# Kernel optimization log

Hardware: AMD Instinct MI355X
Metric: run time of the kernel (lower is better)

The kernel has to match this reference:

```python
import jax, jax.numpy as jnp
import numpy as np

B = 4
N = 300000
GRIDS = [(64, 48, 8), (32, 24, 4), (16, 12, 2), (8, 6, 1)]
W_IMG = 640
EFF_R = 2.0 * (int(0.01 * W_IMG + 2) / W_IMG)  # 0.025, as in source
MAXV = [EFF_R, 2.0 * EFF_R, 2.0 / 24.0, 2.0 / 12.0, 2.0 / 6.0]
CIN = [3, 18, 66, 130, 130]
COUT = [16, 64, 128, 128, 128]
E_CNT = [3600000, 786432, 196608, 24576, 3072]
V_CNT = [N, 98304, 12288, 1536, 192]


def cartesian(pos, src, dst, max_value):
    # PyG Cartesian(norm=True, cat=False, max_value=mv) followed by clamp(0,1)
    cart = pos[dst] - pos[src]
    return jnp.clip(cart / (2.0 * max_value) + 0.5, 0.0, 1.0)


def spline_conv(x, src, dst, pseudo, Wk, Wr, b, num_nodes):
    # SplineConv, kernel_size=2, degree=1 B-spline over 3-D pseudo coords:
    # 8 corner weights, per-edge trilinear basis, mean aggregation + root + bias.
    p, q = pseudo, 1.0 - pseudo
    xs = x[src]  # [E, Cin] gather
    msg = jnp.zeros((src.shape[0], Wk.shape[-1]), x.dtype)
    for s in range(8):
        basis = ((p[:, 0] if s & 1 else q[:, 0])
                 * (p[:, 1] if s & 2 else q[:, 1])
                 * (p[:, 2] if s & 4 else q[:, 2]))
        msg = msg + basis[:, None] * (xs @ Wk[s])
    agg = jax.ops.segment_sum(msg, dst, num_segments=num_nodes)
    deg = jax.ops.segment_sum(jnp.ones((dst.shape[0],), x.dtype), dst, num_segments=num_nodes)
    out = agg / jnp.maximum(deg, 1.0)[:, None] + x @ Wr + b
    return jax.nn.relu(out)


def voxel_pool(x, pos, batch, grid, aggr):
    nx, ny, nt = grid
    ix = jnp.clip(jnp.floor(pos[:, 0] * nx).astype(jnp.int32), 0, nx - 1)
    iy = jnp.clip(jnp.floor(pos[:, 1] * ny).astype(jnp.int32), 0, ny - 1)
    it = jnp.clip(jnp.floor(pos[:, 2] * nt).astype(jnp.int32), 0, nt - 1)
    cluster = ((batch * nx + ix) * ny + iy) * nt + it
    V = B * nx * ny * nt
    ones = jnp.ones((x.shape[0],), x.dtype)
    cnt = jax.ops.segment_sum(ones, cluster, num_segments=V)
    posp = jax.ops.segment_sum(pos, cluster, num_segments=V) / jnp.maximum(cnt, 1.0)[:, None]
    if aggr == 'max':
        xp = jax.ops.segment_max(x, cluster, num_segments=V)
        xp = jnp.where(cnt[:, None] > 0, xp, 0.0)
    else:
        xp = jax.ops.segment_sum(x, cluster, num_segments=V) / jnp.maximum(cnt, 1.0)[:, None]
    batchp = jnp.arange(V, dtype=jnp.int32) // (nx * ny * nt)
    return xp, posp, batchp


def _forward(x, pos, batch, edges, params):
    e0 = edges[0]
    ea = cartesian(pos, e0[0], e0[1], MAXV[0])
    h = jnp.concatenate([x, pos[:, :2]], axis=1)
    Wk, Wr, bb = params[0]
    h = spline_conv(h, e0[0], e0[1], ea, Wk, Wr, bb, x.shape[0])
    h, pos, batch = voxel_pool(h, pos, batch, GRIDS[0], 'max')
    out3 = None
    for i in range(4):
        e = edges[i + 1]
        ea = cartesian(pos, e[0], e[1], MAXV[i + 1])
        h = jnp.concatenate([h, pos[:, :2]], axis=1)
        Wk, Wr, bb = params[i + 1]
        h = spline_conv(h, e[0], e[1], ea, Wk, Wr, bb, pos.shape[0])
        if i == 2:
            out3 = h  # features after layer4 (out3 scale)
        if i < 3:
            h, pos, batch = voxel_pool(h, pos, batch, GRIDS[i + 1], 'max' if i < 2 else 'mean')
    return out3, h


def setup_inputs() -> dict:
    key = jax.random.key(0)
    ks = jax.random.split(key, 40)
    inp = {}
    inp['x'] = jax.random.uniform(ks[0], (N, 1), dtype=jnp.float32)
    inp['pos'] = jax.random.uniform(ks[1], (N, 3), dtype=jnp.float32)
    inp['batch'] = jnp.sort(jax.random.randint(ks[2], (N,), 0, B, dtype=jnp.int32))
    for i in range(5):
        inp[f'e{i}'] = jax.random.randint(ks[3 + i], (2, E_CNT[i]), 0, V_CNT[i], dtype=jnp.int32)
    kidx = 8
    for i in range(5):
        scale = 1.0 / np.sqrt(8.0 * CIN[i])
        inp[f'W{i + 1}'] = scale * jax.random.normal(ks[kidx], (8, CIN[i], COUT[i]), dtype=jnp.float32); kidx += 1
        inp[f'R{i + 1}'] = scale * jax.random.normal(ks[kidx], (CIN[i], COUT[i]), dtype=jnp.float32); kidx += 1
        inp[f'b{i + 1}'] = jnp.zeros((COUT[i],), dtype=jnp.float32)
    return inp


def reference(x, pos, batch, e0, e1, e2, e3, e4,
              W1, R1, b1, W2, R2, b2, W3, R3, b3, W4, R4, b4, W5, R5, b5):
    params = [(W1, R1, b1), (W2, R2, b2), (W3, R3, b3), (W4, R4, b4), (W5, R5, b5)]
    edges = [e0, e1, e2, e3, e4]
    return _forward(x, pos, batch, edges, params)
```

## Files before the change

kernel.cpp:

```cpp
#include <hip/hip_runtime.h>
#include <cstdint>

__device__ __forceinline__ float clamp01f(float v) { return fminf(fmaxf(v, 0.0f), 1.0f); }

__device__ __forceinline__ void basis8(float p0, float p1, float p2, float* bs)
{
    float q0 = 1.f - p0, q1 = 1.f - p1, q2 = 1.f - p2;
    float t00 = q0 * q1, t10 = p0 * q1, t01 = q0 * p1, t11 = p0 * p1;
    bs[0] = t00 * q2; bs[1] = t10 * q2; bs[2] = t01 * q2; bs[3] = t11 * q2;
    bs[4] = t00 * p2; bs[5] = t10 * p2; bs[6] = t01 * p2; bs[7] = t11 * p2;
}

__global__ __launch_bounds__(256) void edge_count_kernel(
    const int* __restrict__ edst, int* __restrict__ cnt, int E)
{
    int e = blockIdx.x * 256 + threadIdx.x;
    if (e < E) atomicAdd(&cnt[__builtin_nontemporal_load(&edst[e])], 1);
}

__global__ __launch_bounds__(256) void edge_scatter_kernel(
    const int* __restrict__ esrc, const int* __restrict__ edst,
    int* __restrict__ off, int* __restrict__ srcs, int E, int rv)
{
    const int lo = (int)(blockIdx.x & 7) * rv;
    const int hi = lo + rv;
    const int base = (int)(blockIdx.x >> 3) << 10;
#pragma unroll
    for (int k = 0; k < 4; ++k) {
        int e = base + (k << 8) + threadIdx.x;
        if (e < E) {
            int d = __builtin_nontemporal_load(&edst[e]);
            if (d >= lo && d < hi) {
                int s = __builtin_nontemporal_load(&esrc[e]);
                int slot = atomicAdd(&off[d], 1);
                srcs[slot] = s;
            }
        }
    }
}

__global__ __launch_bounds__(256) void scan1_kernel(
    const int* __restrict__ cnt, int* __restrict__ off, int* __restrict__ bsum, int V)
{
    __shared__ int lds[4096];
    __shared__ int ssum[256];
    const int t = threadIdx.x;
    const int base = blockIdx.x * 4096;
    for (int i = t; i < 4096; i += 256) {
        int g = base + i;
        lds[i] = (g < V) ? cnt[g] : 0;
    }
    __syncthreads();
    int loc[16];
    int s = 0;
#pragma unroll
    for (int k = 0; k < 16; ++k) { loc[k] = s; s += lds[t * 16 + k]; }
    ssum[t] = s;
    __syncthreads();
    for (int d = 1; d < 256; d <<= 1) {
        int v = (t >= d) ? ssum[t - d] : 0;
        __syncthreads();
        ssum[t] += v;
        __syncthreads();
    }
    const int tbase = (t == 0) ? 0 : ssum[t - 1];
    if (t == 255 && bsum) bsum[blockIdx.x] = ssum[255];
#pragma unroll
    for (int k = 0; k < 16; ++k) lds[t * 16 + k] = tbase + loc[k];
    __syncthreads();
    for (int i = t; i < 4096; i += 256) {
        int g = base + i;
        if (g < V) off[g] = lds[i];
    }
}

__global__ __launch_bounds__(256) void scan_add_kernel(
    int* __restrict__ off, const int* __restrict__ bso, int V)
{
    int g = blockIdx.x * 256 + threadIdx.x;
    if (g < V) off[g] += bso[g >> 12];
}

__global__ __launch_bounds__(256) void bin_count_kernel(
    const int* __restrict__ edst, int* __restrict__ gcnt, int E, int shift)
{
    __shared__ int h[256];
    const int t = threadIdx.x;
    h[t] = 0;
    __syncthreads();
    const int base = blockIdx.x << 12;
#pragma unroll
    for (int k = 0; k < 16; ++k) {
        int e = base + (k << 8) + t;
        if (e < E) {
            int d = __builtin_nontemporal_load(&edst[e]);
            atomicAdd(&h[d >> shift], 1);
        }
    }
    __syncthreads();
    if (h[t]) atomicAdd(&gcnt[t], h[t]);
}

__global__ __launch_bounds__(256) void bin_scatter_kernel(
    const int* __restrict__ esrc, const int* __restrict__ edst,
    int* __restrict__ gcur, int2* __restrict__ st, int E, int shift)
{
    __shared__ int d_l[4096];
    __shared__ int s_l[4096];
    __shared__ int h[256];
    __shared__ int rbase[256];
    const int t = threadIdx.x;
    h[t] = 0;
    __syncthreads();
    const int base = blockIdx.x << 12;
#pragma unroll
    for (int k = 0; k < 16; ++k) {
        int i = (k << 8) + t;
        int e = base + i;
        if (e < E) {
            int d = __builtin_nontemporal_load(&edst[e]);
            int s = __builtin_nontemporal_load(&esrc[e]);
            d_l[i] = d; s_l[i] = s;
            atomicAdd(&h[d >> shift], 1);
        }
    }
    __syncthreads();
    rbase[t] = h[t] ? atomicAdd(&gcur[t], h[t]) : 0;
    h[t] = 0;
    __syncthreads();
#pragma unroll
    for (int k = 0; k < 16; ++k) {
        int i = (k << 8) + t;
        int e = base + i;
        if (e < E) {
            int d = d_l[i];
            int b = d >> shift;
            int r = atomicAdd(&h[b], 1);
            st[rbase[b] + r] = make_int2(d, s_l[i]);
        }
    }
}

__global__ __launch_bounds__(1024) void bucket_csr_kernel(
    const int* __restrict__ gcur, const int* __restrict__ gcnt,
    const int2* __restrict__ st,
    int* __restrict__ cnt, int* __restrict__ off, int* __restrict__ srcs,
    int V, int shift)
{
    __shared__ int h[2048];
    __shared__ int o[2048];
    __shared__ int ps[1024];
    const int t = threadIdx.x;
    const int b = blockIdx.x;
    const int v0 = b << shift;
    const int nv = min(1 << shift, V - v0);
    const int s1 = gcur[b];
    const int s0 = s1 - gcnt[b];
    h[t] = 0; h[t + 1024] = 0;
    __syncthreads();
    for (int i = s0 + t; i < s1; i += 1024)
        atomicAdd(&h[st[i].x - v0], 1);
    __syncthreads();
    int a = h[2 * t], b2 = h[2 * t + 1];
    ps[t] = a + b2;
    __syncthreads();
    for (int d = 1; d < 1024; d <<= 1) {
        int v = (t >= d) ? ps[t - d] : 0;
        __syncthreads();
        ps[t] += v;
        __syncthreads();
    }
    int pb = (t == 0) ? 0 : ps[t - 1];
    o[2 * t] = pb;
    o[2 * t + 1] = pb + a;
    __syncthreads();
    for (int i = t; i < nv; i += 1024) {
        int hv = h[i];
        cnt[v0 + i] = hv;
        off[v0 + i] = s0 + o[i] + hv;
    }
    __syncthreads();
    for (int i = s0 + t; i < s1; i += 1024) {
        int2 e = st[i];
        int r = atomicAdd(&o[e.x - v0], 1);
        srcs[s0 + r] = e.y;
    }
}

__global__ __launch_bounds__(256) void pack_xpos_kernel(
    const float* __restrict__ x, const float* __restrict__ pos,
    float4* __restrict__ xp, int V)
{
    int n = blockIdx.x * 256 + threadIdx.x;
    if (n >= V) return;
    xp[n] = make_float4(x[n], pos[n * 3 + 0], pos[n * 3 + 1], pos[n * 3 + 2]);
}

__device__ __forceinline__ void l1_edge_acc(
    const float4 d, const float4 a, float inv2mv, float ts[8][3])
{
    float p0 = clamp01f((d.y - a.y) * inv2mv + 0.5f);
    float p1 = clamp01f((d.z - a.z) * inv2mv + 0.5f);
    float p2 = clamp01f((d.w - a.w) * inv2mv + 0.5f);
    float bs[8];
    basis8(p0, p1, p2, bs);
#pragma unroll
    for (int s8 = 0; s8 < 8; ++s8) {
        ts[s8][0] += bs[s8] * a.x;
        ts[s8][1] += bs[s8] * a.y;
        ts[s8][2] += bs[s8] * a.z;
    }
}

__global__ __launch_bounds__(256) void l1_fused_kernel(
    const int* __restrict__ off, const int* __restrict__ cnt, const int* __restrict__ srcs,
    const float4* __restrict__ xp,
    const float* __restrict__ Wk, const float* __restrict__ Wr,
    const float* __restrict__ bias, float* __restrict__ out,
    float inv2mv, int V)
{
    __shared__ float sWk[384];
    __shared__ float sWr[48];
    __shared__ float sB[16];
    const int t = threadIdx.x;
    for (int i = t; i < 384; i += 256) sWk[i] = Wk[i];
    if (t < 48) sWr[t] = Wr[t];
    if (t < 16) sB[t] = bias[t];
    __syncthreads();
    const int v = blockIdx.x * 256 + t;
    if (v >= V) return;
    const float4 d = xp[v];
    const int e1 = off[v];
    const int n = cnt[v];
    float ts[8][3];
#pragma unroll
    for (int s8 = 0; s8 < 8; ++s8) { ts[s8][0] = 0.f; ts[s8][1] = 0.f; ts[s8][2] = 0.f; }
    int j = e1 - n;
    for (; j + 3 < e1; j += 4) {
        float4 a0 = xp[srcs[j]];
        float4 a1 = xp[srcs[j + 1]];
        float4 a2 = xp[srcs[j + 2]];
        float4 a3 = xp[srcs[j + 3]];
        l1_edge_acc(d, a0, inv2mv, ts);
        l1_edge_acc(d, a1, inv2mv, ts);
        l1_edge_acc(d, a2, inv2mv, ts);
        l1_edge_acc(d, a3, inv2mv, ts);
    }
    for (; j < e1; ++j)
        l1_edge_acc(d, xp[srcs[j]], inv2mv, ts);
    const float invn = 1.0f / fmaxf((float)n, 1.0f);
    float rr[16];
#pragma unroll
    for (int c = 0; c < 16; ++c) {
        float m = 0.f;
#pragma unroll
        for (int s8 = 0; s8 < 8; ++s8)
            m += ts[s8][0] * sWk[s8 * 48 + c]
               + ts[s8][1] * sWk[s8 * 48 + 16 + c]
               + ts[s8][2] * sWk[s8 * 48 + 32 + c];
        float r = m * invn + d.x * sWr[c] + d.y * sWr[16 + c] + d.z * sWr[32 + c] + sB[c];
        rr[c] = fmaxf(r, 0.0f);
    }
    float4* op = (float4*)(out + (size_t)v * 16);
#pragma unroll
    for (int k = 0; k < 4; ++k)
        op[k] = make_float4(rr[4 * k], rr[4 * k + 1], rr[4 * k + 2], rr[4 * k + 3]);
}

__device__ __forceinline__ void l2_edge_acc(
    const float4 pd, const float4 pa, float fa, int l16, float inv2mv,
    float* accF, float* accP)
{
    float p0 = clamp01f((pd.x - pa.x) * inv2mv + 0.5f);
    float p1 = clamp01f((pd.y - pa.y) * inv2mv + 0.5f);
    float p2 = clamp01f((pd.z - pa.z) * inv2mv + 0.5f);
    float bs[8];
    basis8(p0, p1, p2, bs);
    const float fp = (l16 == 0) ? pa.x : ((l16 == 1) ? pa.y : 0.f);
#pragma unroll
    for (int s8 = 0; s8 < 8; ++s8) {
        accF[s8] += bs[s8] * fa;
        accP[s8] += bs[s8] * fp;
    }
}

template<int NW>
__global__ __launch_bounds__(64 * NW) void tsum16_layer_kernel(
    const int* __restrict__ off, const int* __restrict__ cnt, const int* __restrict__ srcs,
    const float4* __restrict__ pos4, const float* __restrict__ feat,
    const float* __restrict__ Wk, const float* __restrict__ Wr,
    const float* __restrict__ bias, float* __restrict__ out,
    float inv2mv, int V)
{
    __shared__ float tsum[NW][4][18][9];
    const int tid = threadIdx.x;
    const int w = tid >> 6, lane = tid & 63;
    const int q = lane >> 4, l16 = lane & 15;
    const int vbase = (blockIdx.x * NW + w) * 4;
    const int v = vbase + q;

    const float4 pd = pos4[v];
    const int e1 = off[v];
    const int n = cnt[v];
    float accF[8], accP[8];
#pragma unroll
    for (int s8 = 0; s8 < 8; ++s8) { accF[s8] = 0.f; accP[s8] = 0.f; }
    int j = e1 - n;
    for (; j + 3 < e1; j += 4) {
        const int s0 = srcs[j], s1 = srcs[j + 1], s2 = srcs[j + 2], s3 = srcs[j + 3];
        const float4 pa = pos4[s0];
        const float4 pb = pos4[s1];
        const float4 pc = pos4[s2];
        const float4 pe = pos4[s3];
        const float fa = feat[s0 * 16 + l16];
        const float fb = feat[s1 * 16 + l16];
        const float fc = feat[s2 * 16 + l16];
        const float fe = feat[s3 * 16 + l16];
        l2_edge_acc(pd, pa, fa, l16, inv2mv, accF, accP);
        l2_edge_acc(pd, pb, fb, l16, inv2mv, accF, accP);
        l2_edge_acc(pd, pc, fc, l16, inv2mv, accF, accP);
        l2_edge_acc(pd, pe, fe, l16, inv2mv, accF, accP);
    }
    for (; j < e1; ++j) {
        const int s = srcs[j];
        const float4 pa = pos4[s];
        const float fa = feat[s * 16 + l16];
        l2_edge_acc(pd, pa, fa, l16, inv2mv, accF, accP);
    }
#pragma unroll
    for (int s8 = 0; s8 < 8; ++s8)
        tsum[w][q][l16][s8] = accF[s8];
    tsum[w][q][l16][8] = feat[v * 16 + l16];
    if (l16 < 2) {
#pragma unroll
        for (int s8 = 0; s8 < 8; ++s8)
            tsum[w][q][16 + l16][s8] = accP[s8];
        tsum[w][q][16 + l16][8] = (l16 == 0) ? pd.x : pd.y;
    }
    __syncthreads();

    float oA[4], oR[4];
#pragma unroll
    for (int b = 0; b < 4; ++b) { oA[b] = 0.f; oR[b] = 0.f; }
    for (int s8 = 0; s8 < 8; ++s8) {
        const float* W = Wk + (size_t)s8 * 18 * 64;
        for (int ci = 0; ci < 18; ++ci) {
            float wv = W[ci * 64 + lane];
#pragma unroll
            for (int b = 0; b < 4; ++b)
                oA[b] += tsum[w][b][ci][s8] * wv;
        }
    }
    for (int ci = 0; ci < 18; ++ci) {
        float wv = Wr[ci * 64 + lane];
#pragma unroll
        for (int b = 0; b < 4; ++b)
            oR[b] += tsum[w][b][ci][8] * wv;
    }
    const float bi = bias[lane];
#pragma unroll
    for (int b = 0; b < 4; ++b) {
        int vv = vbase + b;
        float invn = 1.0f / fmaxf((float)cnt[vv], 1.0f);
        out[(size_t)vv * 64 + lane] = fmaxf(oA[b] * invn + oR[b] + bi, 0.0f);
    }
}

template<int CINF, int COUT, int NV, int NW, int PMODE>
__global__ __launch_bounds__(64 * NW) void tsum_layer_kernel(
    const int* __restrict__ off, const int* __restrict__ cnt, const int* __restrict__ srcs,
    const float4* __restrict__ pos4, const float* __restrict__ feat,
    const float* __restrict__ Wk, const float* __restrict__ Wr,
    const float* __restrict__ bias, float* __restrict__ out,
    float* __restrict__ hp, float* __restrict__ psum, float* __restrict__ pcnt,
    float inv2mv, int V, int gx, int gy, int gt, int bdiv)
{
    constexpr int CIN = CINF + 2;
    constexpr int NCI = (CIN + 63) / 64;
    constexpr int NCC = COUT / 64;
    __shared__ float tsum[NW][NV][CIN][9];
    __shared__ int scl[NW][NV];
    const int tid = threadIdx.x;
    const int w = tid >> 6, lane = tid & 63;
    const int vbase = (blockIdx.x * NW + w) * NV;

    for (int b = 0; b < NV; ++b) {
        const int v = vbase + b;
        if (v >= V) break;
        const float4 pd = pos4[v];
        float acc[NCI][8];
#pragma unroll
        for (int k = 0; k < NCI; ++k)
#pragma unroll
            for (int s8 = 0; s8 < 8; ++s8) acc[k][s8] = 0.f;
        const int e1 = off[v];
        int j = e1 - cnt[v];
        for (; j + 1 < e1; j += 2) {
            const int s0 = srcs[j], s1 = srcs[j + 1];
            const float4 pa = pos4[s0];
            const float4 pb = pos4[s1];
            float fa[NCI], fb[NCI];
#pragma unroll
            for (int k = 0; k < NCI; ++k) {
                int ci = lane + 64 * k;
                fa[k] = (ci < CINF) ? feat[s0 * CINF + ci]
                       : (ci == CINF ? pa.x : (ci == CINF + 1 ? pa.y : 0.f));
                fb[k] = (ci < CINF) ? feat[s1 * CINF + ci]
                       : (ci == CINF ? pb.x : (ci == CINF + 1 ? pb.y : 0.f));
            }
            float pa0 = clamp01f((pd.x - pa.x) * inv2mv + 0.5f);
            float pa1 = clamp01f((pd.y - pa.y) * inv2mv + 0.5f);
            float pa2 = clamp01f((pd.z - pa.z) * inv2mv + 0.5f);
            float pb0 = clamp01f((pd.x - pb.x) * inv2mv + 0.5f);
            float pb1 = clamp01f((pd.y - pb.y) * inv2mv + 0.5f);
            float pb2 = clamp01f((pd.z - pb.z) * inv2mv + 0.5f);
            float ba[8], bb[8];
            basis8(pa0, pa1, pa2, ba);
            basis8(pb0, pb1, pb2, bb);
#pragma unroll
            for (int s8 = 0; s8 < 8; ++s8)
#pragma unroll
                for (int k = 0; k < NCI; ++k)
                    acc[k][s8] += ba[s8] * fa[k] + bb[s8] * fb[k];
        }
        if (j < e1) {
            const int s = srcs[j];
            const float4 pa = pos4[s];
            float fa[NCI];
#pragma unroll
            for (int k = 0; k < NCI; ++k) {
                int ci = lane + 64 * k;
                fa[k] = (ci < CINF) ? feat[s * CINF + ci]
                       : (ci == CINF ? pa.x : (ci == CINF + 1 ? pa.y : 0.f));
            }
            float p0 = clamp01f((pd.x - pa.x) * inv2mv + 0.5f);
            float p1 = clamp01f((pd.y - pa.y) * inv2mv + 0.5f);
            float p2 = clamp01f((pd.z - pa.z) * inv2mv + 0.5f);
            float bs[8];
            basis8(p0, p1, p2, bs);
#pragma unroll
            for (int s8 = 0; s8 < 8; ++s8)
#pragma unroll
                for (int k = 0; k < NCI; ++k)
                    acc[k][s8] += bs[s8] * fa[k];
        }
#pragma unroll
        for (int k = 0; k < NCI; ++k) {
            int ci = lane + 64 * k;
            if (ci < CIN) {
#pragma unroll
                for (int s8 = 0; s8 < 8; ++s8)
                    tsum[w][b][ci][s8] = acc[k][s8];
                tsum[w][b][ci][8] = (ci < CINF) ? feat[v * CINF + ci]
                                                : (ci == CINF ? pd.x : pd.y);
            }
        }
        if (PMODE != 0 && lane == 0) {
            int bb2 = v / bdiv;
            int ix = min(max((int)floorf(pd.x * (float)gx), 0), gx - 1);
            int iy = min(max((int)floorf(pd.y * (float)gy), 0), gy - 1);
            int it = min(max((int)floorf(pd.z * (float)gt), 0), gt - 1);
            int cl = ((bb2 * gx + ix) * gy + iy) * gt + it;
            scl[w][b] = cl;
            atomicAdd(&psum[cl * 3 + 0], pd.x);
            atomicAdd(&psum[cl * 3 + 1], pd.y);
            atomicAdd(&psum[cl * 3 + 2], pd.z);
            atomicAdd(&pcnt[cl], 1.0f);
        }
    }
    __syncthreads();

    float oA[NV][NCC], oR[NV][NCC];
#pragma unroll
    for (int b = 0; b < NV; ++b)
#pragma unroll
        for (int cc = 0; cc < NCC; ++cc) { oA[b][cc] = 0.f; oR[b][cc] = 0.f; }
    for (int s8 = 0; s8 < 8; ++s8) {
        const float* W = Wk + (size_t)s8 * CIN * COUT;
        for (int ci = 0; ci < CIN; ++ci) {
            float wv[NCC];
#pragma unroll
            for (int cc = 0; cc < NCC; ++cc)
                wv[cc] = W[(size_t)ci * COUT + cc * 64 + lane];
#pragma unroll
            for (int b = 0; b < NV; ++b) {
                float tv = tsum[w][b][ci][s8];
#pragma unroll
                for (int cc = 0; cc < NCC; ++cc) oA[b][cc] += tv * wv[cc];
            }
        }
    }
    for (int ci = 0; ci < CIN; ++ci) {
        float wv[NCC];
#pragma unroll
        for (int cc = 0; cc < NCC; ++cc)
            wv[cc] = Wr[(size_t)ci * COUT + cc * 64 + lane];
#pragma unroll
        for (int b = 0; b < NV; ++b) {
            float tv = tsum[w][b][ci][8];
#pragma unroll
            for (int cc = 0; cc < NCC; ++cc) oR[b][cc] += tv * wv[cc];
        }
    }
    for (int b = 0; b < NV; ++b) {
        int v = vbase + b;
        if (v >= V) break;
        float invn = 1.0f / fmaxf((float)cnt[v], 1.0f);
#pragma unroll
        for (int cc = 0; cc < NCC; ++cc) {
            int c = cc * 64 + lane;
            float val = fmaxf(oA[b][cc] * invn + oR[b][cc] + bias[c], 0.0f);
            if (PMODE == 0 || PMODE == 2)
                out[(size_t)v * COUT + c] = val;
            if (PMODE == 1)
                atomicMax((int*)&hp[(size_t)scl[w][b] * COUT + c], __float_as_int(val));
            if (PMODE == 2)
                atomicAdd(&hp[(size_t)scl[w][b] * COUT + c], val);
        }
    }
}

__global__ __launch_bounds__(256) void pool_cluster_kernel(
    const float* __restrict__ p4, int ofs, const int* __restrict__ batch, int bdiv, int V,
    int nx, int ny, int nt, int* __restrict__ cl, int* __restrict__ cnt)
{
    int n = blockIdx.x * 256 + threadIdx.x;
    if (n >= V) return;
    int b = batch ? batch[n] : (n / bdiv);
    const float* pp = p4 + (size_t)n * 4 + ofs;
    float px = pp[0], py = pp[1], pt = pp[2];
    int ix = (int)floorf(px * (float)nx); ix = min(max(ix, 0), nx - 1);
    int iy = (int)floorf(py * (float)ny); iy = min(max(iy, 0), ny - 1);
    int it = (int)floorf(pt * (float)nt); it = min(max(it, 0), nt - 1);
    int c = ((b * nx + ix) * ny + iy) * nt + it;
    cl[n] = c;
    atomicAdd(&cnt[c], 1);
}

__global__ __launch_bounds__(256) void pool_scatter_kernel(
    const int* __restrict__ cl, int* __restrict__ off, int* __restrict__ order, int V, int rv)
{
    const int lo = (int)(blockIdx.x & 7) * rv;
    const int hi = lo + rv;
    const int base = (int)(blockIdx.x >> 3) << 10;
#pragma unroll
    for (int k = 0; k < 4; ++k) {
        int n = base + (k << 8) + threadIdx.x;
        if (n < V) {
            int c = __builtin_nontemporal_load(&cl[n]);
            if (c >= lo && c < hi) {
                int slot = atomicAdd(&off[c], 1);
                order[slot] = n;
            }
        }
    }
}

template<int COUT>
__global__ __launch_bounds__(256) void staged_pool_kernel(
    const int* __restrict__ order, const int* __restrict__ cl,
    const int* __restrict__ ioff, const int* __restrict__ icnt,
    const float* __restrict__ h, const float* __restrict__ p4, int ofs,
    float* __restrict__ hp, float* __restrict__ psum, int V)
{
    __shared__ float sh[256][COUT + 4];
    __shared__ float sp[256][3];
    __shared__ int scl2[256];
    const int t = threadIdx.x;
    const int w = t >> 6, lane = t & 63;
    const int gbase = blockIdx.x * 256 + w * 64;
    const int slot = gbase + lane;
    int myc = -1;
    if (slot < V) {
        int n = order[slot];
        myc = cl[n];
        const float* hr = h + (size_t)n * COUT;
#pragma unroll
        for (int k = 0; k < COUT / 4; ++k)
            *(float4*)&sh[w * 64 + lane][k * 4] = *(const float4*)&hr[k * 4];
        const float* pp = p4 + (size_t)n * 4 + ofs;
        sp[w * 64 + lane][0] = pp[0];
        sp[w * 64 + lane][1] = pp[1];
        sp[w * 64 + lane][2] = pp[2];
    }
    scl2[w * 64 + lane] = myc;
    __syncthreads();

    if (lane < COUT) {
        const int c = lane;
        const int sb = w * 64;
        int prev = scl2[sb];
        float run = 0.f, rp = 0.f;
        for (int i = 0; i < 64; ++i) {
            int cc = scl2[sb + i];
            if (cc != prev) {
                if (prev >= 0) {
                    int en = ioff[prev];
                    int st = en - icnt[prev];
                    if (st >= gbase && en <= gbase + 64) {
                        hp[(size_t)prev * COUT + c] = run;
                        if (c < 3) psum[prev * 3 + c] = rp;
                    } else {
                        atomicMax((int*)&hp[(size_t)prev * COUT + c], __float_as_int(run));
                        if (c < 3) atomicAdd(&psum[prev * 3 + c], rp);
                    }
                }
                prev = cc; run = 0.f; rp = 0.f;
            }
            if (cc >= 0) {
                run = fmaxf(run, sh[sb + i][c]);
                if (c < 3) rp += sp[sb + i][c];
            }
        }
        if (prev >= 0) {
            int en = ioff[prev];
            int st = en - icnt[prev];
            if (st >= gbase && en <= gbase + 64) {
                hp[(size_t)prev * COUT + c] = run;
                if (c < 3) psum[prev * 3 + c] = rp;
            } else {
                atomicMax((int*)&hp[(size_t)prev * COUT + c], __float_as_int(run));
                if (c < 3) atomicAdd(&psum[prev * 3 + c], rp);
            }
        }
    }
}

__global__ __launch_bounds__(256) void finalize_posI_kernel(
    const float* __restrict__ psum, const int* __restrict__ icnt,
    float4* __restrict__ pos_out, int Vc)
{
    int c = blockIdx.x * 256 + threadIdx.x;
    if (c >= Vc) return;
    float m = fmaxf((float)icnt[c], 1.0f);
    pos_out[c] = make_float4(psum[c * 3 + 0] / m, psum[c * 3 + 1] / m,
                             psum[c * 3 + 2] / m, 0.f);
}

__global__ __launch_bounds__(256) void finalize_pos_kernel(
    const float* __restrict__ psum, const float* __restrict__ pcnt,
    float4* __restrict__ pos_out, int Vc)
{
    int c = blockIdx.x * 256 + threadIdx.x;
    if (c >= Vc) return;
    float m = fmaxf(pcnt[c], 1.0f);
    pos_out[c] = make_float4(psum[c * 3 + 0] / m, psum[c * 3 + 1] / m,
                             psum[c * 3 + 2] / m, 0.f);
}

__global__ __launch_bounds__(256) void finalize_mean_kernel(
    const float* __restrict__ hsum, const float* __restrict__ psum,
    const float* __restrict__ pcnt,
    float* __restrict__ hout, float4* __restrict__ pos_out, int Vc)
{
    int g = blockIdx.x * 256 + threadIdx.x;
    if (g >= Vc * 128) return;
    int c = g >> 7, ch = g & 127;
    float m = fmaxf(pcnt[c], 1.0f);
    hout[g] = hsum[g] / m;
    if (ch == 0)
        pos_out[c] = make_float4(psum[c * 3 + 0] / m, psum[c * 3 + 1] / m,
                                 psum[c * 3 + 2] / m, 0.f);
}

extern "C" void kernel_launch(void* const* d_in, const int* in_sizes, int n_in,
                              void* d_out, int out_size, void* d_ws, size_t ws_size,
                              hipStream_t stream)
{
    (void)in_sizes; (void)n_in; (void)out_size;
    const float* x    = (const float*)d_in[0];
    const float* pos0 = (const float*)d_in[1];
    const int*   bat  = (const int*)d_in[2];
    const int* e1 = (const int*)d_in[3];
    const int* e2 = (const int*)d_in[4];
    const int* e3 = (const int*)d_in[5];
    const int* e4 = (const int*)d_in[6];
    const int* e5 = (const int*)d_in[7];
    const float* W1 = (const float*)d_in[8],  *R1 = (const float*)d_in[9],  *B1 = (const float*)d_in[10];
    const float* W2 = (const float*)d_in[11], *R2 = (const float*)d_in[12], *B2 = (const float*)d_in[13];
    const float* W3 = (const float*)d_in[14], *R3 = (const float*)d_in[15], *B3 = (const float*)d_in[16];
    const float* W4 = (const float*)d_in[17], *R4 = (const float*)d_in[18], *B4 = (const float*)d_in[19];
    const float* W5 = (const float*)d_in[20], *R5 = (const float*)d_in[21], *B5 = (const float*)d_in[22];

    const int E1 = 3600000, E2 = 786432, E3 = 196608, E4 = 24576, E5 = 3072;

    if (ws_size < (size_t)21800000 * sizeof(float)) return;
    float* ws = (float*)d_ws;
    float* P0 = ws;
    float* P1 = ws + 12600000;
    float* P2 = ws + 18900000;
    int*   P3 = (int*)(ws + 20500000);
    float* P4 = ws + 21500000;
    int* GCNT   = P3 + 990000;
    int* GCUR   = P3 + 990256;
    int* SCR_BS = P3 + 999744;
    int* SCR_BO = SCR_BS + 96;

    float* out3 = (float*)d_out;
    float* hfin = (float*)d_out + 196608;

#define MSI(p, ni) hipMemsetAsync((p), 0, (size_t)(ni) * sizeof(int), stream)

#define SCAN(cntp, offp, Vn)                                                                     \
    {                                                                                            \
        int nb_ = ((Vn) + 4095) / 4096;                                                          \
        if (nb_ <= 1) {                                                                          \
            scan1_kernel<<<1, 256, 0, stream>>>((cntp), (offp), nullptr, (Vn));                  \
        } else {                                                                                 \
            scan1_kernel<<<nb_, 256, 0, stream>>>((cntp), (offp), SCR_BS, (Vn));                 \
            scan1_kernel<<<1, 256, 0, stream>>>(SCR_BS, SCR_BO, nullptr, nb_);                   \
            scan_add_kernel<<<((Vn) + 255) / 256, 256, 0, stream>>>((offp), SCR_BO, (Vn));       \
        }                                                                                        \
    }

#define BSORT(cntP, offP, srcP, stP, ep, En, Vn, SHIFT, NB)                                      \
    {                                                                                            \
        MSI(GCNT, 256);                                                                          \
        bin_count_kernel<<<((En) + 4095) / 4096, 256, 0, stream>>>((ep) + (En), GCNT, En, SHIFT);\
        scan1_kernel<<<1, 256, 0, stream>>>(GCNT, GCUR, nullptr, NB);                            \
        bin_scatter_kernel<<<((En) + 4095) / 4096, 256, 0, stream>>>(                            \
            (ep), (ep) + (En), GCUR, stP, En, SHIFT);                                            \
        bucket_csr_kernel<<<NB, 1024, 0, stream>>>(                                              \
            GCUR, GCNT, stP, cntP, offP, srcP, Vn, SHIFT);                                       \
    }

#define ESORT(base, ep, En, Vn)                                                                  \
    int* cnt_ = (base);                                                                          \
    int* off_ = cnt_ + (Vn);                                                                     \
    int* src_ = off_ + (Vn);                                                                     \
    MSI(cnt_, (Vn));                                                                             \
    edge_count_kernel<<<((En) + 255) / 256, 256, 0, stream>>>((ep) + (En), cnt_, En);            \
    SCAN(cnt_, off_, (Vn));                                                                      \
    edge_scatter_kernel<<<8 * (((En) + 1023) / 1024), 256, 0, stream>>>(                         \
        (ep), (ep) + (En), off_, src_, En, (Vn) >> 3)

#define SPOOL(ICLp, IORDp, ICNTp, IOFFp, p4src, ofsv, batp, bdiv, Vn, Vc, NX, NY, NT, COUTV, \
              hsrc, hpool, psumP, posdst)                                                   \
    {                                                                                       \
        MSI(ICNTp, (Vc));                                                                   \
        pool_cluster_kernel<<<((Vn) + 255) / 256, 256, 0, stream>>>(                        \
            p4src, ofsv, batp, bdiv, Vn, NX, NY, NT, ICLp, ICNTp);                          \
        SCAN(ICNTp, IOFFp, (Vc));                                                           \
        pool_scatter_kernel<<<8 * (((Vn) + 1023) / 1024), 256, 0, stream>>>(                \
            ICLp, IOFFp, IORDp, Vn, (Vc) >> 3);                                             \
        MSI(hpool, (size_t)(Vc) * (COUTV));                                                 \
        MSI(psumP, (size_t)(Vc) * 3);                                                       \
        staged_pool_kernel<COUTV><<<((Vn) + 255) / 256, 256, 0, stream>>>(                  \
            IORDp, ICLp, IOFFp, ICNTp, hsrc, p4src, ofsv, hpool, psumP, Vn);                \
        finalize_posI_kernel<<<((Vc) + 255) / 256, 256, 0, stream>>>(                       \
            psumP, ICNTp, (float4*)(posdst), Vc);                                           \
    }

    {
        int* cnt1 = (int*)P0;
        int* off1 = cnt1 + 300000;
        int* src1 = off1 + 300000;
        int2* st1 = (int2*)(src1 + 3600000);
        float4* xp4 = (float4*)(P0 + 11400000);
        BSORT(cnt1, off1, src1, st1, e1, E1, 300000, 11, 147);
        pack_xpos_kernel<<<(300000 + 255) / 256, 256, 0, stream>>>(x, pos0, xp4, 300000);
        l1_fused_kernel<<<(300000 + 255) / 256, 256, 0, stream>>>(
            off1, cnt1, src1, xp4, W1, R1, B1, P1, 20.0f, 300000);
        int* ICL1  = P3;
        int* IORD1 = P3 + 300000;
        int* ICNT1 = P3 + 600000;
        int* IOFF1 = P3 + 698304;
        SPOOL(ICL1, IORD1, ICNT1, IOFF1, (const float*)xp4, 1, bat, 0, 300000, 98304,
              64, 48, 8, 16, P1, P2, P0, P0 + 300000);
    }
    float4* pos2_4 = (float4*)(P0 + 300000);
    {
        int* cnt2 = P3;
        int* off2 = cnt2 + 98304;
        int* src2 = off2 + 98304;
        int2* st2 = (int2*)(P0 + 1000000);
        BSORT(cnt2, off2, src2, st2, e2, E2, 98304, 10, 96);
        tsum16_layer_kernel<4><<<98304 / 16, 256, 0, stream>>>(
            off2, cnt2, src2, pos2_4, P2, W2, R2, B2, P1, 10.0f, 98304);
        int* ICL2  = P3;
        int* IORD2 = P3 + 98304;
        int* ICNT2 = P3 + 196608;
        int* IOFF2 = P3 + 208896;
        SPOOL(ICL2, IORD2, ICNT2, IOFF2, (const float*)pos2_4, 0, nullptr, 24576,
              98304, 12288, 32, 24, 4, 64, P1, P2, P2 + 786432, P4);
    }
    {
        ESORT(P3, e3, E3, 12288);
        float* HP3 = P1;
        float* PS3 = P1 + 196608;
        float* PC3 = P1 + 201216;
        MSI(P1, 202752);
        tsum_layer_kernel<64, 128, 4, 4, 1><<<12288 / 16, 256, 0, stream>>>(
            off_, cnt_, src_, (const float4*)P4, P2, W3, R3, B3, nullptr,
            HP3, PS3, PC3, 6.0f, 12288, 16, 12, 2, 3072);
        finalize_pos_kernel<<<(1536 + 255) / 256, 256, 0, stream>>>(
            PS3, PC3, (float4*)P0, 1536);
    }
    {
        ESORT(P3, e4, E4, 1536);
        float* HS4 = P2;
        float* PS4 = P2 + 24576;
        float* PC4 = P2 + 25152;
        MSI(P2, 25344);
        tsum_layer_kernel<128, 128, 2, 4, 2><<<1536 / 8, 256, 0, stream>>>(
            off_, cnt_, src_, (const float4*)P0, P1, W4, R4, B4, out3,
            HS4, PS4, PC4, 3.0f, 1536, 8, 6, 1, 384);
        finalize_mean_kernel<<<(192 * 128 + 255) / 256, 256, 0, stream>>>(
            HS4, PS4, PC4, P1, (float4*)(P0 + 100000), 192);
    }
    {
        ESORT(P3, e5, E5, 192);
        tsum_layer_kernel<128, 128, 2, 4, 0><<<192 / 8, 256, 0, stream>>>(
            off_, cnt_, src_, (const float4*)(P0 + 100000), P1, W5, R5, B5, hfin,
            nullptr, nullptr, nullptr, 1.5f, 192, 1, 1, 1, 1);
    }
#undef SPOOL
#undef ESORT
#undef BSORT
#undef SCAN
#undef MSI
}
```

Before: 840.9 us.

## Fuse voxel cluster assignment into conv kernels and simplify pseudo-coordinate math

Drops the separate pool_cluster_kernel. Voxel cluster ids and counts are now computed at the end of the layer-1 and layer-2 spline conv kernels, and buffers are relocated so layer 2 does not overwrite the sort buffers. Per-edge pseudo-coordinate math is rewritten as a precomputed destination offset plus one FMA, and the clamp uses fmed3. This saves two launches and a re-read of positions, at the cost of extra atomics inside the conv kernels and slightly different floating-point rounding.

```diff
diff --git a/kernel.cpp b/kernel.cpp
--- a/kernel.cpp
+++ b/kernel.cpp
@@ -1,7 +1,10 @@
 #include <hip/hip_runtime.h>
 #include <cstdint>
 
-__device__ __forceinline__ float clamp01f(float v) { return fminf(fmaxf(v, 0.0f), 1.0f); }
+__device__ __forceinline__ float clamp01f(float v)
+{
+    return __builtin_amdgcn_fmed3f(v, 0.0f, 1.0f);
+}
 
 __device__ __forceinline__ void basis8(float p0, float p1, float p2, float* bs)
 {
@@ -197,11 +200,11 @@
 }
 
 __device__ __forceinline__ void l1_edge_acc(
-    const float4 d, const float4 a, float inv2mv, float ts[8][3])
-{
-    float p0 = clamp01f((d.y - a.y) * inv2mv + 0.5f);
-    float p1 = clamp01f((d.z - a.z) * inv2mv + 0.5f);
-    float p2 = clamp01f((d.w - a.w) * inv2mv + 0.5f);
+    float dx_, float dy_, float dz_, const float4 a, float inv2mv, float ts[8][3])
+{
+    float p0 = clamp01f(fmaf(-inv2mv, a.y, dx_));
+    float p1 = clamp01f(fmaf(-inv2mv, a.z, dy_));
+    float p2 = clamp01f(fmaf(-inv2mv, a.w, dz_));
     float bs[8];
     basis8(p0, p1, p2, bs);
 #pragma unroll
@@ -214,9 +217,10 @@
 
 __global__ __launch_bounds__(256) void l1_fused_kernel(
     const int* __restrict__ off, const int* __restrict__ cnt, const int* __restrict__ srcs,
-    const float4* __restrict__ xp,
+    const float4* __restrict__ xp, const int* __restrict__ bat,
     const float* __restrict__ Wk, const float* __restrict__ Wr,
     const float* __restrict__ bias, float* __restrict__ out,
+    int* __restrict__ icl, int* __restrict__ icnt,
     float inv2mv, int V)
 {
     __shared__ float sWk[384];
@@ -230,6 +234,9 @@
     const int v = blockIdx.x * 256 + t;
     if (v >= V) return;
     const float4 d = xp[v];
+    const float dx_ = fmaf(d.y, inv2mv, 0.5f);
+    const float dy_ = fmaf(d.z, inv2mv, 0.5f);
+    const float dz_ = fmaf(d.w, inv2mv, 0.5f);
     const int e1 = off[v];
     const int n = cnt[v];
     float ts[8][3];
@@ -241,13 +248,13 @@
         float4 a1 = xp[srcs[j + 1]];
         float4 a2 = xp[srcs[j + 2]];
         float4 a3 = xp[srcs[j + 3]];
-        l1_edge_acc(d, a0, inv2mv, ts);
-        l1_edge_acc(d, a1, inv2mv, ts);
-        l1_edge_acc(d, a2, inv2mv, ts);
-        l1_edge_acc(d, a3, inv2mv, ts);
+        l1_edge_acc(dx_, dy_, dz_, a0, inv2mv, ts);
+        l1_edge_acc(dx_, dy_, dz_, a1, inv2mv, ts);
+        l1_edge_acc(dx_, dy_, dz_, a2, inv2mv, ts);
+        l1_edge_acc(dx_, dy_, dz_, a3, inv2mv, ts);
     }
     for (; j < e1; ++j)
-        l1_edge_acc(d, xp[srcs[j]], inv2mv, ts);
+        l1_edge_acc(dx_, dy_, dz_, xp[srcs[j]], inv2mv, ts);
     const float invn = 1.0f / fmaxf((float)n, 1.0f);
     float rr[16];
 #pragma unroll
@@ -265,15 +272,22 @@
 #pragma unroll
     for (int k = 0; k < 4; ++k)
         op[k] = make_float4(rr[4 * k], rr[4 * k + 1], rr[4 * k + 2], rr[4 * k + 3]);
+    int bb = bat[v];
+    int ix = min(max((int)floorf(d.y * 64.f), 0), 63);
+    int iy = min(max((int)floorf(d.z * 48.f), 0), 47);
+    int it = min(max((int)floorf(d.w * 8.f), 0), 7);
+    int cl = ((bb * 64 + ix) * 48 + iy) * 8 + it;
+    icl[v] = cl;
+    atomicAdd(&icnt[cl], 1);
 }
 
 __device__ __forceinline__ void l2_edge_acc(
-    const float4 pd, const float4 pa, float fa, int l16, float inv2mv,
+    float dx_, float dy_, float dz_, const float4 pa, float fa, int l16, float inv2mv,
     float* accF, float* accP)
 {
-    float p0 = clamp01f((pd.x - pa.x) * inv2mv + 0.5f);
-    float p1 = clamp01f((pd.y - pa.y) * inv2mv + 0.5f);
-    float p2 = clamp01f((pd.z - pa.z) * inv2mv + 0.5f);
+    float p0 = clamp01f(fmaf(-inv2mv, pa.x, dx_));
+    float p1 = clamp01f(fmaf(-inv2mv, pa.y, dy_));
+    float p2 = clamp01f(fmaf(-inv2mv, pa.z, dz_));
     float bs[8];
     basis8(p0, p1, p2, bs);
     const float fp = (l16 == 0) ? pa.x : ((l16 == 1) ? pa.y : 0.f);
@@ -290,6 +304,7 @@
     const float4* __restrict__ pos4, const float* __restrict__ feat,
     const float* __restrict__ Wk, const float* __restrict__ Wr,
     const float* __restrict__ bias, float* __restrict__ out,
+    int* __restrict__ icl, int* __restrict__ icnt,
     float inv2mv, int V)
 {
     __shared__ float tsum[NW][4][18][9];
@@ -300,6 +315,9 @@
     const int v = vbase + q;
 
     const float4 pd = pos4[v];
+    const float dx_ = fmaf(pd.x, inv2mv, 0.5f);
+    const float dy_ = fmaf(pd.y, inv2mv, 0.5f);
+    const float dz_ = fmaf(pd.z, inv2mv, 0.5f);
     const int e1 = off[v];
     const int n = cnt[v];
     float accF[8], accP[8];
@@ -316,16 +334,16 @@
         const float fb = feat[s1 * 16 + l16];
         const float fc = feat[s2 * 16 + l16];
         const float fe = feat[s3 * 16 + l16];
-        l2_edge_acc(pd, pa, fa, l16, inv2mv, accF, accP);
-        l2_edge_acc(pd, pb, fb, l16, inv2mv, accF, accP);
-        l2_edge_acc(pd, pc, fc, l16, inv2mv, accF, accP);
-        l2_edge_acc(pd, pe, fe, l16, inv2mv, accF, accP);
+        l2_edge_acc(dx_, dy_, dz_, pa, fa, l16, inv2mv, accF, accP);
+        l2_edge_acc(dx_, dy_, dz_, pb, fb, l16, inv2mv, accF, accP);
+        l2_edge_acc(dx_, dy_, dz_, pc, fc, l16, inv2mv, accF, accP);
+        l2_edge_acc(dx_, dy_, dz_, pe, fe, l16, inv2mv, accF, accP);
     }
     for (; j < e1; ++j) {
         const int s = srcs[j];
         const float4 pa = pos4[s];
         const float fa = feat[s * 16 + l16];
-        l2_edge_acc(pd, pa, fa, l16, inv2mv, accF, accP);
+        l2_edge_acc(dx_, dy_, dz_, pa, fa, l16, inv2mv, accF, accP);
     }
 #pragma unroll
     for (int s8 = 0; s8 < 8; ++s8)
@@ -336,6 +354,15 @@
         for (int s8 = 0; s8 < 8; ++s8)
             tsum[w][q][16 + l16][s8] = accP[s8];
         tsum[w][q][16 + l16][8] = (l16 == 0) ? pd.x : pd.y;
+    }
+    if (l16 == 0) {
+        int bb = v / 24576;
+        int ix = min(max((int)floorf(pd.x * 32.f), 0), 31);
+        int iy = min(max((int)floorf(pd.y * 24.f), 0), 23);
+        int it = min(max((int)floorf(pd.z * 4.f), 0), 3);
+        int cl = ((bb * 32 + ix) * 24 + iy) * 4 + it;
+        icl[v] = cl;
+        atomicAdd(&icnt[cl], 1);
     }
     __syncthreads();
 
@@ -388,6 +415,9 @@
         const int v = vbase + b;
         if (v >= V) break;
         const float4 pd = pos4[v];
+        const float dx_ = fmaf(pd.x, inv2mv, 0.5f);
+        const float dy_ = fmaf(pd.y, inv2mv, 0.5f);
+        const float dz_ = fmaf(pd.z, inv2mv, 0.5f);
         float acc[NCI][8];
 #pragma unroll
         for (int k = 0; k < NCI; ++k)
@@ -408,12 +438,12 @@
                 fb[k] = (ci < CINF) ? feat[s1 * CINF + ci]
                        : (ci == CINF ? pb.x : (ci == CINF + 1 ? pb.y : 0.f));
             }
-            float pa0 = clamp01f((pd.x - pa.x) * inv2mv + 0.5f);
-            float pa1 = clamp01f((pd.y - pa.y) * inv2mv + 0.5f);
-            float pa2 = clamp01f((pd.z - pa.z) * inv2mv + 0.5f);
-            float pb0 = clamp01f((pd.x - pb.x) * inv2mv + 0.5f);
-            float pb1 = clamp01f((pd.y - pb.y) * inv2mv + 0.5f);
-            float pb2 = clamp01f((pd.z - pb.z) * inv2mv + 0.5f);
+            float pa0 = clamp01f(fmaf(-inv2mv, pa.x, dx_));
+            float pa1 = clamp01f(fmaf(-inv2mv, pa.y, dy_));
+            float pa2 = clamp01f(fmaf(-inv2mv, pa.z, dz_));
+            float pb0 = clamp01f(fmaf(-inv2mv, pb.x, dx_));
+            float pb1 = clamp01f(fmaf(-inv2mv, pb.y, dy_));
+            float pb2 = clamp01f(fmaf(-inv2mv, pb.z, dz_));
             float ba[8], bb[8];
             basis8(pa0, pa1, pa2, ba);
             basis8(pb0, pb1, pb2, bb);
@@ -433,9 +463,9 @@
                 fa[k] = (ci < CINF) ? feat[s * CINF + ci]
                        : (ci == CINF ? pa.x : (ci == CINF + 1 ? pa.y : 0.f));
             }
-            float p0 = clamp01f((pd.x - pa.x) * inv2mv + 0.5f);
-            float p1 = clamp01f((pd.y - pa.y) * inv2mv + 0.5f);
-            float p2 = clamp01f((pd.z - pa.z) * inv2mv + 0.5f);
+            float p0 = clamp01f(fmaf(-inv2mv, pa.x, dx_));
+            float p1 = clamp01f(fmaf(-inv2mv, pa.y, dy_));
+            float p2 = clamp01f(fmaf(-inv2mv, pa.z, dz_));
             float bs[8];
             basis8(p0, p1, p2, bs);
 #pragma unroll
@@ -518,23 +548,6 @@
                 atomicAdd(&hp[(size_t)scl[w][b] * COUT + c], val);
         }
     }
-}
-
-__global__ __launch_bounds__(256) void pool_cluster_kernel(
-    const float* __restrict__ p4, int ofs, const int* __restrict__ batch, int bdiv, int V,
-    int nx, int ny, int nt, int* __restrict__ cl, int* __restrict__ cnt)
-{
-    int n = blockIdx.x * 256 + threadIdx.x;
-    if (n >= V) return;
-    int b = batch ? batch[n] : (n / bdiv);
-    const float* pp = p4 + (size_t)n * 4 + ofs;
-    float px = pp[0], py = pp[1], pt = pp[2];
-    int ix = (int)floorf(px * (float)nx); ix = min(max(ix, 0), nx - 1);
-    int iy = (int)floorf(py * (float)ny); iy = min(max(iy, 0), ny - 1);
-    int it = (int)floorf(pt * (float)nt); it = min(max(it, 0), nt - 1);
-    int c = ((b * nx + ix) * ny + iy) * nt + it;
-    cl[n] = c;
-    atomicAdd(&cnt[c], 1);
 }
 
 __global__ __launch_bounds__(256) void pool_scatter_kernel(
@@ -734,12 +747,8 @@
     edge_scatter_kernel<<<8 * (((En) + 1023) / 1024), 256, 0, stream>>>(                         \
         (ep), (ep) + (En), off_, src_, En, (Vn) >> 3)
 
-#define SPOOL(ICLp, IORDp, ICNTp, IOFFp, p4src, ofsv, batp, bdiv, Vn, Vc, NX, NY, NT, COUTV, \
-              hsrc, hpool, psumP, posdst)                                                   \
+#define SPOOL2(ICLp, IORDp, ICNTp, IOFFp, p4src, ofsv, Vn, Vc, COUTV, hsrc, hpool, psumP, posdst) \
     {                                                                                       \
-        MSI(ICNTp, (Vc));                                                                   \
-        pool_cluster_kernel<<<((Vn) + 255) / 256, 256, 0, stream>>>(                        \
-            p4src, ofsv, batp, bdiv, Vn, NX, NY, NT, ICLp, ICNTp);                          \
         SCAN(ICNTp, IOFFp, (Vc));                                                           \
         pool_scatter_kernel<<<8 * (((Vn) + 1023) / 1024), 256, 0, stream>>>(                \
             ICLp, IOFFp, IORDp, Vn, (Vc) >> 3);                                             \
@@ -757,16 +766,17 @@
         int* src1 = off1 + 300000;
         int2* st1 = (int2*)(src1 + 3600000);
         float4* xp4 = (float4*)(P0 + 11400000);
-        BSORT(cnt1, off1, src1, st1, e1, E1, 300000, 11, 147);
-        pack_xpos_kernel<<<(300000 + 255) / 256, 256, 0, stream>>>(x, pos0, xp4, 300000);
-        l1_fused_kernel<<<(300000 + 255) / 256, 256, 0, stream>>>(
-            off1, cnt1, src1, xp4, W1, R1, B1, P1, 20.0f, 300000);
         int* ICL1  = P3;
         int* IORD1 = P3 + 300000;
         int* ICNT1 = P3 + 600000;
         int* IOFF1 = P3 + 698304;
-        SPOOL(ICL1, IORD1, ICNT1, IOFF1, (const float*)xp4, 1, bat, 0, 300000, 98304,
-              64, 48, 8, 16, P1, P2, P0, P0 + 300000);
+        BSORT(cnt1, off1, src1, st1, e1, E1, 300000, 11, 147);
+        pack_xpos_kernel<<<(300000 + 255) / 256, 256, 0, stream>>>(x, pos0, xp4, 300000);
+        MSI(ICNT1, 98304);
+        l1_fused_kernel<<<(300000 + 255) / 256, 256, 0, stream>>>(
+            off1, cnt1, src1, xp4, bat, W1, R1, B1, P1, ICL1, ICNT1, 20.0f, 300000);
+        SPOOL2(ICL1, IORD1, ICNT1, IOFF1, (const float*)xp4, 1, 300000, 98304,
+               16, P1, P2, P0, P0 + 300000);
     }
     float4* pos2_4 = (float4*)(P0 + 300000);
     {
@@ -775,14 +785,15 @@
         int* src2 = off2 + 98304;
         int2* st2 = (int2*)(P0 + 1000000);
         BSORT(cnt2, off2, src2, st2, e2, E2, 98304, 10, 96);
+        int* ICL2  = (int*)(P0 + 1000000);
+        int* ICNT2 = ICL2 + 98304;
+        int* IORD2 = ICNT2 + 12288;
+        int* IOFF2 = IORD2 + 98304;
+        MSI(ICNT2, 12288);
         tsum16_layer_kernel<4><<<98304 / 16, 256, 0, stream>>>(
-            off2, cnt2, src2, pos2_4, P2, W2, R2, B2, P1, 10.0f, 98304);
-        int* ICL2  = P3;
-        int* IORD2 = P3 + 98304;
-        int* ICNT2 = P3 + 196608;
-        int* IOFF2 = P3 + 208896;
-        SPOOL(ICL2, IORD2, ICNT2, IOFF2, (const float*)pos2_4, 0, nullptr, 24576,
-              98304, 12288, 32, 24, 4, 64, P1, P2, P2 + 786432, P4);
+            off2, cnt2, src2, pos2_4, P2, W2, R2, B2, P1, ICL2, ICNT2, 10.0f, 98304);
+        SPOOL2(ICL2, IORD2, ICNT2, IOFF2, (const float*)pos2_4, 0, 98304, 12288,
+               64, P1, P2, P2 + 786432, P4);
     }
     {
         ESORT(P3, e3, E3, 12288);
@@ -814,7 +825,7 @@
             off_, cnt_, src_, (const float4*)(P0 + 100000), P1, W5, R5, B5, hfin,
             nullptr, nullptr, nullptr, 1.5f, 192, 1, 1, 1, 1);
     }
-#undef SPOOL
+#undef SPOOL2
 #undef ESORT
 #undef BSORT
 #undef SCAN
```

New measurement: 829.5 us. About the same (-1.4%).
